# Optimization experiments

Measured on AMD Instinct MI355X. Metric: run time of the kernel, lower is better.

Reference implementation:

```python
import jax, jax.numpy as jnp
import numpy as np

K = 24          # SiFinder.KERNEL_SIZE
SIGMA = 1e-6    # SiFinder.CORR_SIGMA


def setup_inputs() -> dict:
    key = jax.random.key(0)
    k1, k2, k3 = jax.random.split(key, 3)
    H = W = 480
    x_dec = jax.random.normal(k1, (1, 3, H, W), dtype=jnp.float32)
    y_dec = jax.random.normal(k2, (1, 3, H, W), dtype=jnp.float32)
    y = jax.random.normal(k3, (1, 3, H, W), dtype=jnp.float32)
    return {"x_dec": x_dec, "y_dec": y_dec, "y": y}


def _get_x_patches(x_dec):
    # non-overlapping KxK patches, raster order (rows of patches, then cols)
    _, C, H, W = x_dec.shape
    p = x_dec[0].reshape(C, H // K, K, W // K, K)
    return p.transpose(1, 3, 0, 2, 4).reshape(-1, C, K, K)  # (P, C, K, K)


def _conv(img, w):
    # valid cross-correlation, matches F.conv2d
    return jax.lax.conv_general_dilated(
        img, w, window_strides=(1, 1), padding='VALID',
        dimension_numbers=('NCHW', 'OIHW', 'NCHW'))


def _pearson_corr(x_patches, y):
    C = x_patches.shape[1]
    ps = C * K * K  # patch_size
    mean_x = jnp.mean(x_patches, axis=(1, 2, 3))[None, :, None, None]   # (1,P,1,1)
    sum_x2 = jnp.sum(x_patches ** 2, axis=(1, 2, 3))[None, :, None, None]
    ones = jnp.ones((1, C, K, K), y.dtype)
    sum_y = _conv(y, ones)            # (1,1,H',W'); torch builds P identical channels
    xy = _conv(y, x_patches)          # (1,P,H',W')
    numer = xy / ps - mean_x * sum_y / ps
    den_x = sum_x2 / ps - mean_x ** 2
    den_y = _conv(y ** 2, ones) / ps - sum_y ** 2 / ps ** 2
    return (2 * numer + SIGMA) / (jnp.abs(den_x) + jnp.abs(den_y) + SIGMA)


def _forward(x_dec, y_dec, y):
    x_patches = _get_x_patches(x_dec)
    corr = _pearson_corr(x_patches, y_dec)          # (1, P, H', W')
    _, P, Hc, Wc = corr.shape
    idx = jnp.argmax(corr[0].reshape(P, Hc * Wc), axis=-1)
    rows, cols = idx // Wc, idx % Wc
    # roi_align(boxes=[-0.5+c, -0.5+r, ...], out=KxK, sampling_ratio=-1) samples
    # exactly at integer pixel centers -> reduces to an exact patch gather from y.
    C = y.shape[1]
    def take(r, c):
        return jax.lax.dynamic_slice(y[0], (0, r, c), (C, K, K))
    patches = jax.vmap(take)(rows, cols)            # (P, C, K, K)
    # nn.Fold with stride==kernel: stitch non-overlapping patches back to image
    H, W = x_dec.shape[2], x_dec.shape[3]
    img = patches.reshape(H // K, W // K, C, K, K).transpose(2, 0, 3, 1, 4)
    return img.reshape(1, C, H, W)


def reference(x_dec, y_dec, y):
    return _forward(x_dec, y_dec, y)
```

## Files before the change

### kernel.cpp

```cpp
#include <hip/hip_runtime.h>
#include <stdint.h>

#define HW    480
#define KS    24
#define CH    3
#define HO    457
#define NPOS  (HO*HO)
#define NP    400
#define PS    (CH*KS*KS)
#define SIG   1e-6f
#define NSQ   54
#define NMT   13
#define NIY   115
#define NGRP  (NIY*8*4)
#define MAXF  16384
#define RGRID 4096
#define DELTA 4e-3f
#define QS    28.0f
#define IS2   (1.0f/(QS*QS))
#define PLS   2592
#define CHS   (4*PLS)
#define LDSZ  (3*CHS)

typedef __attribute__((ext_vector_type(4)))  int  int4v;
typedef __attribute__((ext_vector_type(16))) int  int16v;
typedef unsigned int uint;
typedef unsigned char uchar;
typedef unsigned long long ull;

static __device__ __forceinline__ char q8(float v) {
    float s = rintf(v * QS);
    s = fminf(127.f, fmaxf(-127.f, s));
    return (char)(int)s;
}
static __device__ __forceinline__ uint mono(float f) {
    uint u = __float_as_uint(f);
    return (u & 0x80000000u) ? ~u : (u | 0x80000000u);
}
static __device__ __forceinline__ float unmono(uint u) {
    uint b = (u & 0x80000000u) ? (u & 0x7fffffffu) : ~u;
    return __uint_as_float(b);
}

__global__ void fat1_k(const float* __restrict__ x, const float* __restrict__ yd,
                       float* __restrict__ Wp, char* __restrict__ yq,
                       float* __restrict__ cs, float* __restrict__ cs2) {
    int b = blockIdx.x;
    if (b < 2700) {
        int t = b * 256 + threadIdx.x;
        int p = t / PS, e = t - p * PS;
        int c = e / (KS * KS);
        int r = (e / KS) % KS;
        int w = e % KS;
        int pr = p / 20, pc = p - pr * 20;
        Wp[t] = x[c * HW * HW + (pr * KS + r) * HW + (pc * KS + w)];
    } else if (b < 5400) {
        int t = (b - 2700) * 256 + threadIdx.x;
        yq[t] = q8(yd[t]);
    } else {
        int t = (b - 5400) * 256 + threadIdx.x;
        if (t >= HO * HW) return;
        int i = t / HW, w = t - i * HW;
        float s = 0.f, s2 = 0.f;
        for (int c = 0; c < CH; c++) {
            const float* base = yd + c * HW * HW + i * HW + w;
            for (int dh = 0; dh < KS; dh++) {
                float v = base[dh * HW];
                s += v; s2 += v * v;
            }
        }
        cs[t] = s; cs2[t] = s2;
    }
}

__global__ void fat2_k(const float* __restrict__ Wp,
                       const float* __restrict__ cs, const float* __restrict__ cs2,
                       float* __restrict__ meanX, float* __restrict__ denXa,
                       char* __restrict__ Aq,
                       float* __restrict__ sumY, float* __restrict__ denYa,
                       uint* __restrict__ cnt, ull* __restrict__ best) {
    __shared__ float shs[4], shs2[4];
    int b = blockIdx.x;
    if (b < 400) {
        int p = b;
        if (threadIdx.x == 1) best[p] = 0ull;
        if (b == 0 && threadIdx.x == 2) *cnt = 0u;
        float s = 0.f, s2 = 0.f;
        for (int e = threadIdx.x; e < PS; e += 256) {
            float v = Wp[p * PS + e];
            s += v; s2 += v * v;
        }
        for (int o = 32; o > 0; o >>= 1) { s += __shfl_down(s, o); s2 += __shfl_down(s2, o); }
        int lane = threadIdx.x & 63, wv = threadIdx.x >> 6;
        if (lane == 0) { shs[wv] = s; shs2[wv] = s2; }
        __syncthreads();
        if (threadIdx.x == 0) {
            float S = shs[0] + shs[1] + shs[2] + shs[3];
            float S2 = shs2[0] + shs2[1] + shs2[2] + shs2[3];
            float m = S / (float)PS;
            meanX[p] = m;
            denXa[p] = fabsf(S2 / (float)PS - m * m);
        }
    } else if (b < 3208) {
        int id = (b - 400) * 256 + threadIdx.x;
        int e    = id & 15;
        int lane = (id >> 4) & 63;
        int f    = id >> 10;
        int s    = f % NSQ;
        int mtg  = f / NSQ;
        int kk = s * 32 + (lane >> 5) * 16 + e;
        int p  = mtg * 32 + (lane & 31);
        float v = (p < NP) ? Wp[p * PS + kk] : 0.f;
        Aq[id] = q8(v);
    } else {
        int t = (b - 3208) * 256 + threadIdx.x;
        if (t >= NPOS) return;
        int i = t / HO, j = t - i * HO;
        const float* r  = cs  + i * HW + j;
        const float* r2 = cs2 + i * HW + j;
        float s = 0.f, s2 = 0.f;
        for (int d = 0; d < KS; d++) { s += r[d]; s2 += r2[d]; }
        sumY[t] = s;
        float ips = 1.0f / (float)PS;
        denYa[t] = fabsf(s2 * ips - (s * ips) * (s * ips));
    }
}

template<int MT>
static __device__ __forceinline__ void corr1_body(
        const int mt0,
        const char* __restrict__ yq, const char* __restrict__ Aq,
        const float* __restrict__ meanX, const float* __restrict__ denXa,
        const float* __restrict__ sumY, const float* __restrict__ denYa,
        uint* __restrict__ table, uchar* __restrict__ S) {
    const int tid  = threadIdx.x;
    const int lane = tid & 63;
    const int g    = tid >> 6;
    const int n    = lane & 31;
    const int kha  = lane >> 5;
    const int jx   = blockIdx.x;
    const int iy   = blockIdx.y;
    const int j0   = 64 * jx;
    const int i0   = 4 * iy;
    const int i    = i0 + g;

    for (int it = tid; it < 3 * 27 * 6; it += 256) {
        int ch  = it / 162, rem = it - ch * 162;
        int row = rem / 6,  gb  = rem - row * 6;
        int yr  = i0 + row;
        int gj  = j0 + gb * 16;
        uint d[6];
        if (yr < HW && gj + 24 <= HW) {
            const uchar* src = (const uchar*)yq + ((size_t)(ch * HW + yr)) * HW + gj;
            uint4 a = *(const uint4*)src;
            uint2 bb = *(const uint2*)(src + 16);
            d[0] = a.x; d[1] = a.y; d[2] = a.z; d[3] = a.w; d[4] = bb.x; d[5] = bb.y;
        } else {
            uchar tmp[24];
#pragma unroll
            for (int e = 0; e < 24; e++) {
                int col = gj + e;
                tmp[e] = (yr < HW && col < HW)
                       ? ((const uchar*)yq)[((size_t)(ch * HW + yr)) * HW + col] : (uchar)0;
            }
            const uint* tp = (const uint*)tmp;
#pragma unroll
            for (int e = 0; e < 6; e++) d[e] = tp[e];
        }
        int base = ch * CHS + row * 96 + gb * 16;
        uint s0 = (d[0] >> 16) | (d[1] << 16);
        uint s1 = (d[1] >> 16) | (d[2] << 16);
        uint s2 = (d[2] >> 16) | (d[3] << 16);
        uint s3 = (d[3] >> 16) | (d[4] << 16);
        uint s4 = (d[4] >> 16) | (d[5] << 16);
        *(uint4*)&S[base]           = make_uint4(d[0], d[1], d[2], d[3]);
        *(uint4*)&S[base + PLS]     = make_uint4(s0, s1, s2, s3);
        *(uint4*)&S[base + 2*PLS]   = make_uint4(d[1], d[2], d[3], d[4]);
        *(uint4*)&S[base + 3*PLS]   = make_uint4(s1, s2, s3, s4);
    }
    __syncthreads();

    const int olo[3] = { kha ? 16  : 0,   kha ? 192 : 104, kha ? 296 : 208 };
    const int ohi[3] = { kha ? 96  : 8,   kha ? 200 : 112, kha ? 304 : 288 };

    const uchar* Sp = S + (n & 3) * PLS + ((2 * n) & ~7) + g * 96;

    const char* Ab0 = Aq + ((size_t)mt0 * NSQ << 10) + lane * 16;
    const char* Ab[2] = { Ab0, Ab0 + ((size_t)NSQ << 10) };

    int16v acc[MT][2];
#pragma unroll
    for (int mt = 0; mt < MT; mt++)
#pragma unroll
        for (int t = 0; t < 2; t++) acc[mt][t] = (int16v)0;

    int4v av[2][MT][3];
#pragma unroll
    for (int mt = 0; mt < MT; mt++)
#pragma unroll
        for (int u = 0; u < 3; u++)
            av[0][mt][u] = *(const int4v*)(Ab[mt] + (u << 10));

#pragma unroll
    for (int Q = 0; Q < 18; Q++) {
        const int cur = Q & 1;
        if (Q < 17) {
#pragma unroll
            for (int mt = 0; mt < MT; mt++)
#pragma unroll
                for (int u = 0; u < 3; u++)
                    av[cur ^ 1][mt][u] =
                        *(const int4v*)(Ab[mt] + (((Q + 1) * 3 + u) << 10));
        }
        const int IQ = (Q / 6) * CHS + (Q % 6) * 384;
#pragma unroll
        for (int u = 0; u < 3; u++) {
            uint2 wl0 = *(const uint2*)(Sp + IQ + olo[u]);
            uint2 wl1 = *(const uint2*)(Sp + IQ + olo[u] + 8);
            uint2 wh0 = *(const uint2*)(Sp + IQ + ohi[u]);
            uint2 wh1 = *(const uint2*)(Sp + IQ + ohi[u] + 8);
            int4v bv0, bv1;
            bv0.x = (int)wl0.x; bv0.y = (int)wl0.y;
            bv0.z = (int)wh0.x; bv0.w = (int)wh0.y;
            bv1.x = (int)__builtin_amdgcn_perm(wl0.y, wl0.x, 0x04030201u);
            bv1.y = (int)__builtin_amdgcn_perm(wl1.x, wl0.y, 0x04030201u);
            bv1.z = (int)__builtin_amdgcn_perm(wh0.y, wh0.x, 0x04030201u);
            bv1.w = (int)__builtin_amdgcn_perm(wh1.x, wh0.y, 0x04030201u);
#pragma unroll
            for (int mt = 0; mt < MT; mt++) {
                acc[mt][0] = __builtin_amdgcn_mfma_i32_32x32x32_i8(
                                 av[cur][mt][u], bv0, acc[mt][0], 0, 0, 0);
                acc[mt][1] = __builtin_amdgcn_mfma_i32_32x32x32_i8(
                                 av[cur][mt][u], bv1, acc[mt][1], 0, 0, 0);
            }
        }
    }

    const int grp = (iy * 8 + jx) * 4 + g;
    const float c2 = 2.0f / (float)PS;
    const bool iok = i < HO;
    float sYv[2], rDv[2];
#pragma unroll
    for (int t = 0; t < 2; t++) {
        int j = j0 + 2 * n + t;
        bool ok = iok && (j < HO);
        sYv[t] = ok ? sumY[i * HO + j] : 0.f;
        rDv[t] = ok ? denYa[i * HO + j] : 0.f;
    }
    const bool jv0 = iok && (j0 + 2 * n + 0 < HO);
    const bool jv1 = iok && (j0 + 2 * n + 1 < HO);
#pragma unroll
    for (int mt = 0; mt < MT; mt++) {
        const int pbase = (mt0 + mt) * 32;
#pragma unroll
        for (int r = 0; r < 16; r++) {
            int p = pbase + (r & 3) + 8 * (r >> 2) + 4 * kha;
            bool pok = p < NP;
            float mX = pok ? meanX[p] : 0.f;
            float dX = pok ? denXa[p] : 0.f;
            float num[2], den[2];
#pragma unroll
            for (int t = 0; t < 2; t++) {
                bool ok = t ? jv1 : jv0;
                if (ok) {
                    float xy = (float)acc[mt][t][r] * IS2;
                    num[t] = fmaf(-mX, sYv[t], xy) * c2 + SIG;
                    den[t] = dX + rDv[t] + SIG;
                } else {
                    num[t] = -3.0e38f;
                    den[t] = 1.0f;
                }
            }
            bool pick1 = num[1] * den[0] > num[0] * den[1];
            float nn = pick1 ? num[1] : num[0];
            float dd = pick1 ? den[1] : den[0];
            float bu = nn * __builtin_amdgcn_rcpf(dd);
#pragma unroll
            for (int o = 1; o < 32; o <<= 1)
                bu = fmaxf(bu, __shfl_xor(bu, o));
            if (n == 0 && pok) table[p * NGRP + grp] = mono(bu);
        }
    }
}

__launch_bounds__(256, 3)
__global__ void corr1_k(const char* __restrict__ yq, const char* __restrict__ Aq,
                        const float* __restrict__ meanX, const float* __restrict__ denXa,
                        const float* __restrict__ sumY, const float* __restrict__ denYa,
                        uint* __restrict__ table) {
    __shared__ __align__(16) uchar S[LDSZ];
    if (blockIdx.z == 6)
        corr1_body<1>(12, yq, Aq, meanX, denXa, sumY, denYa, table, S);
    else
        corr1_body<2>(2 * blockIdx.z, yq, Aq, meanX, denXa, sumY, denYa, table, S);
}

__global__ void flag_k(const uint* __restrict__ table,
                       uint* __restrict__ flags, uint* __restrict__ cnt) {
    __shared__ uint sm[4];
    __shared__ float sthr;
    int p = blockIdx.x;
    uint m = 0;
    for (int g = threadIdx.x; g < NGRP; g += 256) {
        uint v = table[p * NGRP + g];
        m = v > m ? v : m;
    }
    for (int o = 32; o > 0; o >>= 1) { uint ot = __shfl_down(m, o); m = ot > m ? ot : m; }
    int lane = threadIdx.x & 63, wv = threadIdx.x >> 6;
    if (lane == 0) sm[wv] = m;
    __syncthreads();
    if (threadIdx.x == 0) {
        uint mm = max(max(sm[0], sm[1]), max(sm[2], sm[3]));
        sthr = unmono(mm) - DELTA;
    }
    __syncthreads();
    float thr = sthr;
    for (int g = threadIdx.x; g < NGRP; g += 256) {
        if (unmono(table[p * NGRP + g]) >= thr) {
            uint idx = atomicAdd(cnt, 1u);
            if (idx < MAXF) flags[idx] = (uint)(p * NGRP + g);
        }
    }
}

__launch_bounds__(64)
__global__ void rescore_k(const float* __restrict__ Wp, const float* __restrict__ y_dec,
                          const float* __restrict__ meanX, const float* __restrict__ denXa,
                          const float* __restrict__ sumY, const float* __restrict__ denYa,
                          const uint* __restrict__ flags, const uint* __restrict__ cnt,
                          ull* __restrict__ best) {
    uint nflag = *cnt; if (nflag > MAXF) nflag = MAXF;
    for (uint fb = blockIdx.x; fb < nflag; fb += RGRID) {
        uint f = flags[fb];
        int p = f / NGRP, grp = f - p * NGRP;
        int g = grp & 3, bj = grp >> 2;
        int jx = bj & 7, iy = bj >> 3;
        int i = 4 * iy + g;
        int j = 64 * jx + threadIdx.x;
        ull pk = 0;
        if (i < HO && j < HO) {
            float dot = 0.f;
            const float* wr = Wp + p * PS;
            for (int c = 0; c < CH; c++)
                for (int kh = 0; kh < KS; kh++) {
                    const float* yr = y_dec + ((c * HW) + i + kh) * HW + j;
                    const float* wk = wr + (c * KS + kh) * KS;
#pragma unroll
                    for (int kw = 0; kw < KS; kw++) dot += wk[kw] * yr[kw];
                }
            float corr = (2.0f * (dot - meanX[p] * sumY[i * HO + j]) * (1.0f / (float)PS) + SIG)
                       / (denXa[p] + denYa[i * HO + j] + SIG);
            uint idx = (uint)(i * HO + j);
            pk = ((ull)mono(corr) << 32) | (uint)(~idx);
        }
        for (int o = 32; o > 0; o >>= 1) { ull ot = __shfl_down(pk, o); pk = ot > pk ? ot : pk; }
        if (threadIdx.x == 0) atomicMax(&best[p], pk);
    }
}

__global__ void gather_k(const float* __restrict__ y,
                         const ull* __restrict__ best,
                         float* __restrict__ out) {
    int p = blockIdx.x;
    uint idx = ~((uint)(best[p] & 0xFFFFFFFFull));
    int r = idx / HO, cc = idx - r * HO;
    int pr = p / 20, pc = p - pr * 20;
    for (int e = threadIdx.x; e < PS; e += 256) {
        int c = e / (KS * KS);
        int kh = (e / KS) % KS;
        int kw = e % KS;
        out[c * HW * HW + (pr * KS + kh) * HW + (pc * KS + kw)] =
            y[c * HW * HW + (r + kh) * HW + (cc + kw)];
    }
}

extern "C" void kernel_launch(void* const* d_in, const int* in_sizes, int n_in,
                              void* d_out, int out_size, void* d_ws, size_t ws_size,
                              hipStream_t stream) {
    const float* x_dec = (const float*)d_in[0];
    const float* y_dec = (const float*)d_in[1];
    const float* y     = (const float*)d_in[2];
    float* out = (float*)d_out;

    char* ws = (char*)d_ws;
    size_t off = 0;
    auto carve = [&](size_t bytes) -> void* {
        void* p = ws + off;
        off += (bytes + 255) & ~(size_t)255;
        return p;
    };
    float*  Wp    = (float*)carve((size_t)NP * PS * 4);
    char*   yq    = (char*)carve((size_t)CH * HW * HW);
    char*   Aq    = (char*)carve((size_t)NMT * NSQ * 1024);
    float*  cs    = (float*)carve((size_t)HO * HW * 4);
    float*  cs2   = (float*)carve((size_t)HO * HW * 4);
    float*  sumY  = (float*)carve((size_t)NPOS * 4);
    float*  denYa = (float*)carve((size_t)NPOS * 4);
    float*  meanX = (float*)carve((size_t)NP * 4);
    float*  denXa = (float*)carve((size_t)NP * 4);
    uint*   table = (uint*)carve((size_t)NP * NGRP * 4);
    uint*   flags = (uint*)carve((size_t)MAXF * 4);
    uint*   cnt   = (uint*)carve(256);
    ull*    best  = (ull*)carve((size_t)NP * 8);

    fat1_k<<<6257, 256, 0, stream>>>(x_dec, y_dec, Wp, yq, cs, cs2);
    fat2_k<<<4024, 256, 0, stream>>>(Wp, cs, cs2, meanX, denXa, Aq, sumY, denYa, cnt, best);

    dim3 grid(8, NIY, 7);
    corr1_k<<<grid, 256, 0, stream>>>(yq, Aq, meanX, denXa, sumY, denYa, table);

    flag_k<<<NP, 256, 0, stream>>>(table, flags, cnt);
    rescore_k<<<RGRID, 64, 0, stream>>>(Wp, y_dec, meanX, denXa, sumY, denYa, flags, cnt, best);

    gather_k<<<NP, 256, 0, stream>>>(y, best, out);
}
```

Baseline: 364.8 us.

## Vectorize box sums, share LDS staging across tiles, split flag pass, widen rescore blocks

Column sums now use float4 loads and row sums compute four outputs per thread from registers. The correlation kernel stages the int8 y tile into LDS once and runs two M-tile bodies per block, cutting the z grid from 7 to 4. It also raises wave priority around the MFMA section. The flag kernel is split into a parallel max pass with an atomicMax and a threshold pass over 8 slices per patch. Rescore runs four waves per block. The aim is less redundant staging, more parallelism in the small kernels and fewer launches' worth of idle hardware, at the cost of an extra kernel launch and more work per corr block.

Result: no change. 365.0 us (+0.0%).

```diff
diff --git a/kernel.cpp b/kernel.cpp
--- a/kernel.cpp
+++ b/kernel.cpp
@@ -14,7 +14,7 @@
 #define NIY   115
 #define NGRP  (NIY*8*4)
 #define MAXF  16384
-#define RGRID 4096
+#define RGB   1024
 #define DELTA 4e-3f
 #define QS    28.0f
 #define IS2   (1.0f/(QS*QS))
@@ -59,17 +59,21 @@
         yq[t] = q8(yd[t]);
     } else {
         int t = (b - 5400) * 256 + threadIdx.x;
-        if (t >= HO * HW) return;
-        int i = t / HW, w = t - i * HW;
-        float s = 0.f, s2 = 0.f;
+        if (t >= HO * 120) return;
+        int i = t / 120, w4 = (t - i * 120) * 4;
+        float4 s  = make_float4(0.f, 0.f, 0.f, 0.f);
+        float4 s2 = make_float4(0.f, 0.f, 0.f, 0.f);
         for (int c = 0; c < CH; c++) {
-            const float* base = yd + c * HW * HW + i * HW + w;
+            const float* base = yd + c * HW * HW + i * HW + w4;
             for (int dh = 0; dh < KS; dh++) {
-                float v = base[dh * HW];
-                s += v; s2 += v * v;
+                float4 v = *(const float4*)(base + dh * HW);
+                s.x += v.x; s.y += v.y; s.z += v.z; s.w += v.w;
+                s2.x += v.x * v.x; s2.y += v.y * v.y;
+                s2.z += v.z * v.z; s2.w += v.w * v.w;
             }
         }
-        cs[t] = s; cs2[t] = s2;
+        *(float4*)(cs  + i * HW + w4) = s;
+        *(float4*)(cs2 + i * HW + w4) = s2;
     }
 }
 
@@ -78,12 +82,14 @@
                        float* __restrict__ meanX, float* __restrict__ denXa,
                        char* __restrict__ Aq,
                        float* __restrict__ sumY, float* __restrict__ denYa,
-                       uint* __restrict__ cnt, ull* __restrict__ best) {
+                       uint* __restrict__ cnt, ull* __restrict__ best,
+                       uint* __restrict__ pmax) {
     __shared__ float shs[4], shs2[4];
     int b = blockIdx.x;
     if (b < 400) {
         int p = b;
         if (threadIdx.x == 1) best[p] = 0ull;
+        if (threadIdx.x == 3) pmax[p] = 0u;
         if (b == 0 && threadIdx.x == 2) *cnt = 0u;
         float s = 0.f, s2 = 0.f;
         for (int e = threadIdx.x; e < PS; e += 256) {
@@ -114,36 +120,31 @@
         Aq[id] = q8(v);
     } else {
         int t = (b - 3208) * 256 + threadIdx.x;
-        if (t >= NPOS) return;
-        int i = t / HO, j = t - i * HO;
-        const float* r  = cs  + i * HW + j;
-        const float* r2 = cs2 + i * HW + j;
-        float s = 0.f, s2 = 0.f;
-        for (int d = 0; d < KS; d++) { s += r[d]; s2 += r2[d]; }
-        sumY[t] = s;
+        if (t >= HO * 115) return;
+        int i = t / 115, j4 = (t - i * 115) * 4;
+        float c1[27], c2v[27];
+#pragma unroll
+        for (int d = 0; d < 27; d++) {
+            c1[d]  = cs [i * HW + j4 + d];
+            c2v[d] = cs2[i * HW + j4 + d];
+        }
         float ips = 1.0f / (float)PS;
-        denYa[t] = fabsf(s2 * ips - (s * ips) * (s * ips));
-    }
-}
-
-template<int MT>
-static __device__ __forceinline__ void corr1_body(
-        const int mt0,
-        const char* __restrict__ yq, const char* __restrict__ Aq,
-        const float* __restrict__ meanX, const float* __restrict__ denXa,
-        const float* __restrict__ sumY, const float* __restrict__ denYa,
-        uint* __restrict__ table, uchar* __restrict__ S) {
-    const int tid  = threadIdx.x;
-    const int lane = tid & 63;
-    const int g    = tid >> 6;
-    const int n    = lane & 31;
-    const int kha  = lane >> 5;
-    const int jx   = blockIdx.x;
-    const int iy   = blockIdx.y;
-    const int j0   = 64 * jx;
-    const int i0   = 4 * iy;
-    const int i    = i0 + g;
-
+#pragma unroll
+        for (int jj = 0; jj < 4; jj++) {
+            int j = j4 + jj;
+            if (j >= HO) break;
+            float s = 0.f, s2 = 0.f;
+#pragma unroll
+            for (int d = 0; d < KS; d++) { s += c1[jj + d]; s2 += c2v[jj + d]; }
+            sumY[i * HO + j] = s;
+            denYa[i * HO + j] = fabsf(s2 * ips - (s * ips) * (s * ips));
+        }
+    }
+}
+
+static __device__ __forceinline__ void stage_all(uchar* __restrict__ S,
+                                                 const char* __restrict__ yq,
+                                                 int i0, int j0, int tid) {
     for (int it = tid; it < 3 * 27 * 6; it += 256) {
         int ch  = it / 162, rem = it - ch * 162;
         int row = rem / 6,  gb  = rem - row * 6;
@@ -178,7 +179,25 @@
         *(uint4*)&S[base + 2*PLS]   = make_uint4(d[1], d[2], d[3], d[4]);
         *(uint4*)&S[base + 3*PLS]   = make_uint4(s1, s2, s3, s4);
     }
-    __syncthreads();
+}
+
+template<int MT>
+static __device__ __forceinline__ void corr1_body(
+        const int mt0,
+        const char* __restrict__ Aq,
+        const float* __restrict__ meanX, const float* __restrict__ denXa,
+        const float* __restrict__ sumY, const float* __restrict__ denYa,
+        uint* __restrict__ table, const uchar* __restrict__ S) {
+    const int tid  = threadIdx.x;
+    const int lane = tid & 63;
+    const int g    = tid >> 6;
+    const int n    = lane & 31;
+    const int kha  = lane >> 5;
+    const int jx   = blockIdx.x;
+    const int iy   = blockIdx.y;
+    const int j0   = 64 * jx;
+    const int i0   = 4 * iy;
+    const int i    = i0 + g;
 
     const int olo[3] = { kha ? 16  : 0,   kha ? 192 : 104, kha ? 296 : 208 };
     const int ohi[3] = { kha ? 96  : 8,   kha ? 200 : 112, kha ? 304 : 288 };
@@ -213,6 +232,7 @@
                         *(const int4v*)(Ab[mt] + (((Q + 1) * 3 + u) << 10));
         }
         const int IQ = (Q / 6) * CHS + (Q % 6) * 384;
+        __builtin_amdgcn_s_setprio(1);
 #pragma unroll
         for (int u = 0; u < 3; u++) {
             uint2 wl0 = *(const uint2*)(Sp + IQ + olo[u]);
@@ -234,6 +254,7 @@
                                  av[cur][mt][u], bv1, acc[mt][1], 0, 0, 0);
             }
         }
+        __builtin_amdgcn_s_setprio(0);
     }
 
     const int grp = (iy * 8 + jx) * 4 + g;
@@ -289,33 +310,34 @@
                         const float* __restrict__ sumY, const float* __restrict__ denYa,
                         uint* __restrict__ table) {
     __shared__ __align__(16) uchar S[LDSZ];
-    if (blockIdx.z == 6)
-        corr1_body<1>(12, yq, Aq, meanX, denXa, sumY, denYa, table, S);
-    else
-        corr1_body<2>(2 * blockIdx.z, yq, Aq, meanX, denXa, sumY, denYa, table, S);
-}
-
-__global__ void flag_k(const uint* __restrict__ table,
-                       uint* __restrict__ flags, uint* __restrict__ cnt) {
-    __shared__ uint sm[4];
-    __shared__ float sthr;
-    int p = blockIdx.x;
+    stage_all(S, yq, 4 * blockIdx.y, 64 * blockIdx.x, threadIdx.x);
+    __syncthreads();
+    if (blockIdx.z == 3) {
+        corr1_body<1>(12, Aq, meanX, denXa, sumY, denYa, table, S);
+    } else {
+        corr1_body<2>(4 * blockIdx.z,     Aq, meanX, denXa, sumY, denYa, table, S);
+        corr1_body<2>(4 * blockIdx.z + 2, Aq, meanX, denXa, sumY, denYa, table, S);
+    }
+}
+
+__global__ void flagmax_k(const uint* __restrict__ table, uint* __restrict__ pmax) {
+    int p = blockIdx.x, sl = blockIdx.y;
+    int g0 = sl * 460;
     uint m = 0;
-    for (int g = threadIdx.x; g < NGRP; g += 256) {
+    for (int g = g0 + threadIdx.x; g < g0 + 460; g += 256) {
         uint v = table[p * NGRP + g];
         m = v > m ? v : m;
     }
     for (int o = 32; o > 0; o >>= 1) { uint ot = __shfl_down(m, o); m = ot > m ? ot : m; }
-    int lane = threadIdx.x & 63, wv = threadIdx.x >> 6;
-    if (lane == 0) sm[wv] = m;
-    __syncthreads();
-    if (threadIdx.x == 0) {
-        uint mm = max(max(sm[0], sm[1]), max(sm[2], sm[3]));
-        sthr = unmono(mm) - DELTA;
-    }
-    __syncthreads();
-    float thr = sthr;
-    for (int g = threadIdx.x; g < NGRP; g += 256) {
+    if ((threadIdx.x & 63) == 0) atomicMax(&pmax[p], m);
+}
+
+__global__ void flag2_k(const uint* __restrict__ table, const uint* __restrict__ pmax,
+                        uint* __restrict__ flags, uint* __restrict__ cnt) {
+    int p = blockIdx.x, sl = blockIdx.y;
+    int g0 = sl * 460;
+    float thr = unmono(pmax[p]) - DELTA;
+    for (int g = g0 + threadIdx.x; g < g0 + 460; g += 256) {
         if (unmono(table[p * NGRP + g]) >= thr) {
             uint idx = atomicAdd(cnt, 1u);
             if (idx < MAXF) flags[idx] = (uint)(p * NGRP + g);
@@ -323,20 +345,21 @@
     }
 }
 
-__launch_bounds__(64)
+__launch_bounds__(256)
 __global__ void rescore_k(const float* __restrict__ Wp, const float* __restrict__ y_dec,
                           const float* __restrict__ meanX, const float* __restrict__ denXa,
                           const float* __restrict__ sumY, const float* __restrict__ denYa,
                           const uint* __restrict__ flags, const uint* __restrict__ cnt,
                           ull* __restrict__ best) {
     uint nflag = *cnt; if (nflag > MAXF) nflag = MAXF;
-    for (uint fb = blockIdx.x; fb < nflag; fb += RGRID) {
+    const int wv = threadIdx.x >> 6, ln = threadIdx.x & 63;
+    for (uint fb = blockIdx.x * 4 + wv; fb < nflag; fb += 4 * RGB) {
         uint f = flags[fb];
         int p = f / NGRP, grp = f - p * NGRP;
         int g = grp & 3, bj = grp >> 2;
         int jx = bj & 7, iy = bj >> 3;
         int i = 4 * iy + g;
-        int j = 64 * jx + threadIdx.x;
+        int j = 64 * jx + ln;
         ull pk = 0;
         if (i < HO && j < HO) {
             float dot = 0.f;
@@ -354,7 +377,7 @@
             pk = ((ull)mono(corr) << 32) | (uint)(~idx);
         }
         for (int o = 32; o > 0; o >>= 1) { ull ot = __shfl_down(pk, o); pk = ot > pk ? ot : pk; }
-        if (threadIdx.x == 0) atomicMax(&best[p], pk);
+        if (ln == 0) atomicMax(&best[p], pk);
     }
 }
 
@@ -402,15 +425,20 @@
     uint*   flags = (uint*)carve((size_t)MAXF * 4);
     uint*   cnt   = (uint*)carve(256);
     ull*    best  = (ull*)carve((size_t)NP * 8);
-
-    fat1_k<<<6257, 256, 0, stream>>>(x_dec, y_dec, Wp, yq, cs, cs2);
-    fat2_k<<<4024, 256, 0, stream>>>(Wp, cs, cs2, meanX, denXa, Aq, sumY, denYa, cnt, best);
-
-    dim3 grid(8, NIY, 7);
+    uint*   pmax  = (uint*)carve((size_t)NP * 4);
+
+    fat1_k<<<5615, 256, 0, stream>>>(x_dec, y_dec, Wp, yq, cs, cs2);
+    fat2_k<<<3414, 256, 0, stream>>>(Wp, cs, cs2, meanX, denXa, Aq, sumY, denYa,
+                                     cnt, best, pmax);
+
+    dim3 grid(8, NIY, 4);
     corr1_k<<<grid, 256, 0, stream>>>(yq, Aq, meanX, denXa, sumY, denYa, table);
 
-    flag_k<<<NP, 256, 0, stream>>>(table, flags, cnt);
-    rescore_k<<<RGRID, 64, 0, stream>>>(Wp, y_dec, meanX, denXa, sumY, denYa, flags, cnt, best);
+    dim3 fgrid(NP, 8);
+    flagmax_k<<<fgrid, 256, 0, stream>>>(table, pmax);
+    flag2_k<<<fgrid, 256, 0, stream>>>(table, pmax, flags, cnt);
+    rescore_k<<<RGB, 256, 0, stream>>>(Wp, y_dec, meanX, denXa, sumY, denYa,
+                                       flags, cnt, best);
 
     gather_k<<<NP, 256, 0, stream>>>(y, best, out);
 }
```
